# Kernel tuning notes

Measured on AMD Instinct MI355X. Metric: run time of the kernel, lower is better.

Reference implementation:

```python
import jax, jax.numpy as jnp
import numpy as np

B, N, D = 8, 2048, 512

def setup_inputs() -> dict:
    key = jax.random.key(0)
    k1, k2, k3, k4, k5 = jax.random.split(key, 5)
    s = 1.0 / np.sqrt(D)
    return {
        "x": jax.random.normal(k1, (B, N, D), dtype=jnp.float32),
        "w_qkv": jax.random.normal(k2, (D, 3 * D), dtype=jnp.float32) * s,
        "b_qkv": jax.random.normal(k3, (3 * D,), dtype=jnp.float32) * 0.01,
        "w_fc": jax.random.normal(k4, (D, D), dtype=jnp.float32) * s,
        "b_fc": jax.random.normal(k5, (D,), dtype=jnp.float32) * 0.01,
    }

def reference(x, w_qkv, b_qkv, w_fc, b_fc):
    scale = 1.0 / (x.shape[-1] ** 0.5)
    qkv = x @ w_qkv + b_qkv                      # [B, N, 3D]
    q, k, v = jnp.split(qkv, 3, axis=-1)         # each [B, N, D]
    attn = jnp.einsum("bnd,bmd->bnm", q, k) * scale
    attn = jax.nn.softmax(attn, axis=-1)
    out = jnp.einsum("bnm,bmd->bnd", attn, v)
    return out @ w_fc + b_fc + x
```

## Files before the change

kernel.cpp:

```cpp
#include <hip/hip_runtime.h>
#include <stdint.h>

typedef unsigned short u16;
typedef unsigned int u32;
typedef __attribute__((ext_vector_type(8))) short short8;
typedef __attribute__((ext_vector_type(4))) float f32x4;
typedef __attribute__((ext_vector_type(8))) unsigned short u16x8;
typedef __attribute__((ext_vector_type(4))) float float4_t;

__device__ __forceinline__ float b2f(u16 u) { return __uint_as_float(((u32)u) << 16); }
__device__ __forceinline__ u16 f2b(float f) {
  u32 u = __float_as_uint(f);
  u += 0x7fffu + ((u >> 16) & 1u);
  return (u16)(u >> 16);
}

typedef const __attribute__((address_space(1))) void* gas_t;
typedef __attribute__((address_space(3))) void* las_t;
__device__ __forceinline__ void gl_lds16(const void* g, void* l) {
  __builtin_amdgcn_global_load_lds((gas_t)(uintptr_t)g, (las_t)(u32)(uintptr_t)l, 16, 0, 0);
}
__device__ __forceinline__ void barrier_pin() {
  __builtin_amdgcn_sched_barrier(0);
  __builtin_amdgcn_s_barrier();
  __builtin_amdgcn_sched_barrier(0);
}
__device__ __forceinline__ void lgkm0_pin() {
  asm volatile("s_waitcnt lgkmcnt(0)" ::: "memory");
  __builtin_amdgcn_sched_barrier(0);
}

__global__ __launch_bounds__(256) void cvt_f2b_kernel(const float* __restrict__ src,
                                                      u16* __restrict__ dst, long n) {
  long i = ((long)blockIdx.x * 256 + threadIdx.x) * 8;
  if (i >= n) return;
  float4_t v0 = *(const float4_t*)(src + i);
  float4_t v1 = *(const float4_t*)(src + i + 4);
  u16x8 o;
#pragma unroll
  for (int j = 0; j < 4; ++j) { o[j] = f2b(v0[j]); o[4 + j] = f2b(v1[j]); }
  *(u16x8*)(dst + i) = o;
}

__global__ __launch_bounds__(256) void tr_cvt2(const float* __restrict__ w1,
                                               u16* __restrict__ d1,
                                               const float* __restrict__ w2,
                                               u16* __restrict__ d2) {
  const int zz = blockIdx.z;
  if (zz == 1 && blockIdx.x >= 16) return;
  const float* src = zz ? w2 : w1;
  u16* dst = zz ? d2 : d1;
  const int C = zz ? 512 : 1536;
  const int R = 512;
  __shared__ float t[32][33];
  const int bx = blockIdx.x * 32;
  const int by = blockIdx.y * 32;
  const int tx = threadIdx.x & 31, ty = threadIdx.x >> 5;
#pragma unroll
  for (int i = 0; i < 32; i += 8)
    t[ty + i][tx] = src[(long)(by + ty + i) * C + bx + tx];
  __syncthreads();
#pragma unroll
  for (int i = 0; i < 32; i += 8)
    dst[(long)(bx + ty + i) * R + by + tx] = f2b(t[tx][ty + i]);
}

__global__ __launch_bounds__(512) void tr_v(const u16* __restrict__ qkv,
                                            u16* __restrict__ vt) {
  __shared__ u16 t[64][66];
  const int b = blockIdx.z;
  const int r0 = blockIdx.x * 64;
  const int d0 = blockIdx.y * 64;
  const int tr = threadIdx.x >> 3;
  const int tc = (threadIdx.x & 7) * 8;
  *(u16x8*)&t[tr][tc] =
      *(const u16x8*)&qkv[((long)b * 2048 + r0 + tr) * 1536 + 1024 + d0 + tc];
  __syncthreads();
  u16x8 o;
#pragma unroll
  for (int j = 0; j < 8; ++j) o[j] = t[tc + j][tr];
  *(u16x8*)&vt[((long)b * 512 + d0 + tr) * 2048 + r0 + tc] = o;
}

template <bool OUT_F32, bool BIAS, bool RES, bool EXP_EPI, bool ROWSUM_ST, bool DIVROW>
__global__ __launch_bounds__(512, 4)
void gemm128(const u16* __restrict__ A, const u16* __restrict__ Bt, void* __restrict__ Cv,
             const float* __restrict__ bias, const float* __restrict__ res,
             float* __restrict__ lglob, const float* __restrict__ lin,
             int K, int lda, int ldb, int ldc,
             long aStride, long bStride, long cStride, float alpha) {
  __shared__ u16 As[2][128 * 64];
  __shared__ u16 Bs[2][128 * 64];
  const int tid = threadIdx.x;
  const int wid = tid >> 6, lane = tid & 63;
  const int wr = wid >> 2, wc = wid & 3;
  const int lr = lane & 15, lg = lane >> 4;

  const int gx = gridDim.x, gy = gridDim.y;
  int id = (blockIdx.z * gy + blockIdx.y) * gx + blockIdx.x;
  const int nwg = gx * gy * gridDim.z;
  id = (id & 7) * (nwg >> 3) + (id >> 3);
  const int bxi = id % gx;
  const int t2 = id / gx;
  const int byi = t2 % gy;
  const long z = t2 / gy;

  A += z * aStride;
  Bt += z * bStride;
  const int by = byi * 128;
  const int bx = bxi * 128;

  const bool do_l = ROWSUM_ST && (bxi == 0);

  f32x4 acc[4][2] = {};
  f32x4 acc_l[4] = {};
  short8 ah[4][2], bh[2][2];
  short8 ones;
#pragma unroll
  for (int j = 0; j < 8; ++j) ones[j] = (short)0x3F80;

  const int w8l = wid * 8 + (lane >> 3);
  const int scol_src = ((lane & 7) ^ (lane >> 3)) * 8;
  const int scol_lin = (lane & 7) * 8;
  const int nT = K >> 6;
  const int sx = lane & 7;

  auto stage = [&](int kt) {
    const int bb = kt & 1;
    const long kc = (long)kt * 64 + scol_src;
#pragma unroll
    for (int r = 0; r < 2; ++r) {
      const int row = r * 64 + w8l;
      gl_lds16(A + (long)(by + row) * lda + kc, &As[bb][row * 64 + scol_lin]);
    }
#pragma unroll
    for (int r = 0; r < 2; ++r) {
      const int row = r * 64 + w8l;
      gl_lds16(Bt + (long)(bx + row) * ldb + kc, &Bs[bb][row * 64 + scol_lin]);
    }
  };

  stage(0);
  asm volatile("s_waitcnt vmcnt(0)" ::: "memory");
  barrier_pin();

  for (int T = 0; T < nT; ++T) {
    const int bb = T & 1;
    const bool more = (T + 1) < nT;
    if (more) stage(T + 1);
#pragma unroll
    for (int mi = 0; mi < 4; ++mi)
#pragma unroll
      for (int ks = 0; ks < 2; ++ks)
        ah[mi][ks] = *(const short8*)&As[bb][(wr * 64 + mi * 16 + lr) * 64 +
                                             (((ks * 4 + lg) ^ sx) * 8)];
#pragma unroll
    for (int n = 0; n < 2; ++n)
#pragma unroll
      for (int ks = 0; ks < 2; ++ks)
        bh[n][ks] = *(const short8*)&Bs[bb][(wc * 32 + n * 16 + lr) * 64 +
                                            (((ks * 4 + lg) ^ sx) * 8)];
    lgkm0_pin();
    __builtin_amdgcn_s_setprio(1);
#pragma unroll
    for (int mi = 0; mi < 4; ++mi)
#pragma unroll
      for (int n = 0; n < 2; ++n)
#pragma unroll
        for (int ks = 0; ks < 2; ++ks)
          acc[mi][n] = __builtin_amdgcn_mfma_f32_16x16x32_bf16(
              ah[mi][ks], bh[n][ks], acc[mi][n], 0, 0, 0);
    if constexpr (ROWSUM_ST) {
      if (do_l && wc == 0) {
#pragma unroll
        for (int mi = 0; mi < 4; ++mi)
#pragma unroll
          for (int ks = 0; ks < 2; ++ks)
            acc_l[mi] = __builtin_amdgcn_mfma_f32_16x16x32_bf16(
                ah[mi][ks], ones, acc_l[mi], 0, 0, 0);
      }
    }
    __builtin_amdgcn_s_setprio(0);
    if (more) asm volatile("s_waitcnt vmcnt(0)" ::: "memory");
    barrier_pin();
  }

  if constexpr (ROWSUM_ST) {
    if (do_l && wc == 0 && lr == 0) {
#pragma unroll
      for (int mi = 0; mi < 4; ++mi)
#pragma unroll
        for (int j = 0; j < 4; ++j)
          lglob[z * 2048 + by + wr * 64 + mi * 16 + lg * 4 + j] = acc_l[mi][j];
    }
  }

  if constexpr (EXP_EPI) {
    u16* C = (u16*)Cv + z * cStride;
#pragma unroll
    for (int mi = 0; mi < 4; ++mi)
#pragma unroll
      for (int ni = 0; ni < 2; ++ni)
#pragma unroll
        for (int j = 0; j < 4; ++j) {
          const long row = by + wr * 64 + mi * 16 + lg * 4 + j;
          const int col = bx + wc * 32 + ni * 16 + lr;
          C[row * (long)ldc + col] = f2b(exp2f(acc[mi][ni][j] * alpha));
        }
  } else if constexpr (OUT_F32) {
    float* C = (float*)Cv + z * cStride;
#pragma unroll
    for (int mi = 0; mi < 4; ++mi)
#pragma unroll
      for (int j = 0; j < 4; ++j) {
        const long row = by + wr * 64 + mi * 16 + lg * 4 + j;
        float invl = 1.0f;
        if constexpr (DIVROW) invl = 1.0f / lin[row];
#pragma unroll
        for (int ni = 0; ni < 2; ++ni) {
          const int col = bx + wc * 32 + ni * 16 + lr;
          float v = acc[mi][ni][j] * alpha;
          if constexpr (DIVROW) v = acc[mi][ni][j] * invl;
          if (BIAS) v += bias[col];
          if (RES) v += res[row * (long)ldc + col];
          C[row * (long)ldc + col] = v;
        }
      }
  } else {
    u16* C = (u16*)Cv + z * cStride;
#pragma unroll
    for (int mi = 0; mi < 4; ++mi)
#pragma unroll
      for (int ni = 0; ni < 2; ++ni)
#pragma unroll
        for (int j = 0; j < 4; ++j) {
          const long row = by + wr * 64 + mi * 16 + lg * 4 + j;
          const int col = bx + wc * 32 + ni * 16 + lr;
          float v = acc[mi][ni][j] * alpha;
          if (BIAS) v += bias[col];
          C[row * (long)ldc + col] = f2b(v);
        }
  }
}

extern "C" void kernel_launch(void* const* d_in, const int* in_sizes, int n_in,
                              void* d_out, int out_size, void* d_ws, size_t ws_size,
                              hipStream_t stream) {
  const float* x = (const float*)d_in[0];
  const float* w_qkv = (const float*)d_in[1];
  const float* b_qkv = (const float*)d_in[2];
  const float* w_fc = (const float*)d_in[3];
  const float* b_fc = (const float*)d_in[4];
  float* out = (float*)d_out;

  char* ws = (char*)d_ws;
  const long MT = 16384;
  u16* xb = (u16*)(ws);
  u16* wqkvT = (u16*)(ws + 16777216);
  u16* wfcT = (u16*)(ws + 18350080);
  u16* qkv = (u16*)(ws + 18874368);
  u16* vt = (u16*)(ws + 69206016);
  u16* S = (u16*)(ws + 85983232);
  u16* attn = xb;
  float* lvec = (float*)(ws + 16777216);

  const float alpha2 = 0.04419417382415922f * 1.4426950408889634f;

  cvt_f2b_kernel<<<4096, 256, 0, stream>>>(x, xb, MT * 512);
  tr_cvt2<<<dim3(48, 16, 2), 256, 0, stream>>>(w_qkv, wqkvT, w_fc, wfcT);

  gemm128<false, true, false, false, false, false><<<dim3(12, 128, 1), 512, 0, stream>>>(
      xb, wqkvT, qkv, b_qkv, nullptr, nullptr, nullptr,
      512, 512, 512, 1536, 0, 0, 0, 1.0f);

  tr_v<<<dim3(32, 8, 8), 512, 0, stream>>>(qkv, vt);

  gemm128<false, false, false, true, false, false><<<dim3(16, 16, 8), 512, 0, stream>>>(
      qkv, qkv + 512, S, nullptr, nullptr, nullptr, nullptr,
      512, 1536, 1536, 2048,
      (long)2048 * 1536, (long)2048 * 1536, (long)2048 * 2048, alpha2);

  gemm128<false, false, false, false, true, false><<<dim3(4, 16, 8), 512, 0, stream>>>(
      S, vt, attn, nullptr, nullptr, lvec, nullptr,
      2048, 2048, 2048, 512,
      (long)2048 * 2048, (long)512 * 2048, (long)2048 * 512, 1.0f);

  gemm128<true, true, true, false, false, true><<<dim3(4, 128, 1), 512, 0, stream>>>(
      attn, wfcT, out, b_fc, x, nullptr, lvec,
      512, 512, 512, 512, 0, 0, 0, 1.0f);
}
```

Baseline: 160.3 us.

## Switch GEMM tiles to 32x32x16 MFMA and merge preprocessing kernels

Each wave's 64x32 sub-tile now uses two 32x32x16 bf16 MFMA accumulators instead of eight 16x16x32 ones. This cuts the MFMA instruction count and the number of LDS fragment reads per k-step, and the epilogue row/column mapping is rewritten to match the 32x32 output layout. Separately, the x conversion and the weight transpose-convert kernels are merged into one launch to save launch overhead. The risk is a different LDS bank access pattern and a less coalesced epilogue, where each thread now writes 16 scattered rows per column.

```diff
diff --git a/kernel.cpp b/kernel.cpp
--- a/kernel.cpp
+++ b/kernel.cpp
@@ -4,7 +4,7 @@
 typedef unsigned short u16;
 typedef unsigned int u32;
 typedef __attribute__((ext_vector_type(8))) short short8;
-typedef __attribute__((ext_vector_type(4))) float f32x4;
+typedef __attribute__((ext_vector_type(16))) float f32x16;
 typedef __attribute__((ext_vector_type(8))) unsigned short u16x8;
 typedef __attribute__((ext_vector_type(4))) float float4_t;
 
@@ -30,31 +30,36 @@
   __builtin_amdgcn_sched_barrier(0);
 }
 
-__global__ __launch_bounds__(256) void cvt_f2b_kernel(const float* __restrict__ src,
-                                                      u16* __restrict__ dst, long n) {
-  long i = ((long)blockIdx.x * 256 + threadIdx.x) * 8;
-  if (i >= n) return;
-  float4_t v0 = *(const float4_t*)(src + i);
-  float4_t v1 = *(const float4_t*)(src + i + 4);
-  u16x8 o;
-#pragma unroll
-  for (int j = 0; j < 4; ++j) { o[j] = f2b(v0[j]); o[4 + j] = f2b(v1[j]); }
-  *(u16x8*)(dst + i) = o;
-}
-
-__global__ __launch_bounds__(256) void tr_cvt2(const float* __restrict__ w1,
-                                               u16* __restrict__ d1,
-                                               const float* __restrict__ w2,
-                                               u16* __restrict__ d2) {
-  const int zz = blockIdx.z;
-  if (zz == 1 && blockIdx.x >= 16) return;
+__global__ __launch_bounds__(256) void preprocess(const float* __restrict__ x,
+                                                  u16* __restrict__ xb,
+                                                  const float* __restrict__ w1,
+                                                  u16* __restrict__ d1,
+                                                  const float* __restrict__ w2,
+                                                  u16* __restrict__ d2) {
+  const int id = blockIdx.x;
+  if (id < 4096) {
+    long i = ((long)id * 256 + threadIdx.x) * 8;
+    float4_t v0 = *(const float4_t*)(x + i);
+    float4_t v1 = *(const float4_t*)(x + i + 4);
+    u16x8 o;
+#pragma unroll
+    for (int j = 0; j < 4; ++j) { o[j] = f2b(v0[j]); o[4 + j] = f2b(v1[j]); }
+    *(u16x8*)(xb + i) = o;
+    return;
+  }
+  const int rid = id - 4096;
+  const int zz = rid / 768;
+  const int rem = rid - zz * 768;
+  const int bxx = rem % 48;
+  const int byy = rem / 48;
+  if (zz == 1 && bxx >= 16) return;
   const float* src = zz ? w2 : w1;
   u16* dst = zz ? d2 : d1;
   const int C = zz ? 512 : 1536;
   const int R = 512;
   __shared__ float t[32][33];
-  const int bx = blockIdx.x * 32;
-  const int by = blockIdx.y * 32;
+  const int bx = bxx * 32;
+  const int by = byy * 32;
   const int tx = threadIdx.x & 31, ty = threadIdx.x >> 5;
 #pragma unroll
   for (int i = 0; i < 32; i += 8)
@@ -94,7 +99,7 @@
   const int tid = threadIdx.x;
   const int wid = tid >> 6, lane = tid & 63;
   const int wr = wid >> 2, wc = wid & 3;
-  const int lr = lane & 15, lg = lane >> 4;
+  const int l31 = lane & 31, lg2 = lane >> 5;
 
   const int gx = gridDim.x, gy = gridDim.y;
   int id = (blockIdx.z * gy + blockIdx.y) * gx + blockIdx.x;
@@ -112,9 +117,9 @@
 
   const bool do_l = ROWSUM_ST && (bxi == 0);
 
-  f32x4 acc[4][2] = {};
-  f32x4 acc_l[4] = {};
-  short8 ah[4][2], bh[2][2];
+  f32x16 acc[2] = {};
+  f32x16 acc_l[2] = {};
+  short8 ah[2][4], bh[4];
   short8 ones;
 #pragma unroll
   for (int j = 0; j < 8; ++j) ones[j] = (short)0x3F80;
@@ -149,35 +154,31 @@
     const bool more = (T + 1) < nT;
     if (more) stage(T + 1);
 #pragma unroll
-    for (int mi = 0; mi < 4; ++mi)
-#pragma unroll
-      for (int ks = 0; ks < 2; ++ks)
-        ah[mi][ks] = *(const short8*)&As[bb][(wr * 64 + mi * 16 + lr) * 64 +
-                                             (((ks * 4 + lg) ^ sx) * 8)];
-#pragma unroll
-    for (int n = 0; n < 2; ++n)
-#pragma unroll
-      for (int ks = 0; ks < 2; ++ks)
-        bh[n][ks] = *(const short8*)&Bs[bb][(wc * 32 + n * 16 + lr) * 64 +
-                                            (((ks * 4 + lg) ^ sx) * 8)];
+    for (int mf = 0; mf < 2; ++mf)
+#pragma unroll
+      for (int kb = 0; kb < 4; ++kb)
+        ah[mf][kb] = *(const short8*)&As[bb][(wr * 64 + mf * 32 + l31) * 64 +
+                                             (((kb * 2 + lg2) ^ sx) * 8)];
+#pragma unroll
+    for (int kb = 0; kb < 4; ++kb)
+      bh[kb] = *(const short8*)&Bs[bb][(wc * 32 + l31) * 64 +
+                                       (((kb * 2 + lg2) ^ sx) * 8)];
     lgkm0_pin();
     __builtin_amdgcn_s_setprio(1);
 #pragma unroll
-    for (int mi = 0; mi < 4; ++mi)
-#pragma unroll
-      for (int n = 0; n < 2; ++n)
-#pragma unroll
-        for (int ks = 0; ks < 2; ++ks)
-          acc[mi][n] = __builtin_amdgcn_mfma_f32_16x16x32_bf16(
-              ah[mi][ks], bh[n][ks], acc[mi][n], 0, 0, 0);
+    for (int kb = 0; kb < 4; ++kb)
+#pragma unroll
+      for (int mf = 0; mf < 2; ++mf)
+        acc[mf] = __builtin_amdgcn_mfma_f32_32x32x16_bf16(
+            ah[mf][kb], bh[kb], acc[mf], 0, 0, 0);
     if constexpr (ROWSUM_ST) {
       if (do_l && wc == 0) {
 #pragma unroll
-        for (int mi = 0; mi < 4; ++mi)
-#pragma unroll
-          for (int ks = 0; ks < 2; ++ks)
-            acc_l[mi] = __builtin_amdgcn_mfma_f32_16x16x32_bf16(
-                ah[mi][ks], ones, acc_l[mi], 0, 0, 0);
+        for (int kb = 0; kb < 4; ++kb)
+#pragma unroll
+          for (int mf = 0; mf < 2; ++mf)
+            acc_l[mf] = __builtin_amdgcn_mfma_f32_32x32x16_bf16(
+                ah[mf][kb], ones, acc_l[mf], 0, 0, 0);
       }
     }
     __builtin_amdgcn_s_setprio(0);
@@ -185,61 +186,52 @@
     barrier_pin();
   }
 
+  const int col = bx + wc * 32 + l31;
   if constexpr (ROWSUM_ST) {
-    if (do_l && wc == 0 && lr == 0) {
-#pragma unroll
-      for (int mi = 0; mi < 4; ++mi)
-#pragma unroll
-        for (int j = 0; j < 4; ++j)
-          lglob[z * 2048 + by + wr * 64 + mi * 16 + lg * 4 + j] = acc_l[mi][j];
+    if (do_l && wc == 0 && l31 == 0) {
+#pragma unroll
+      for (int mf = 0; mf < 2; ++mf)
+#pragma unroll
+        for (int reg = 0; reg < 16; ++reg)
+          lglob[z * 2048 + by + wr * 64 + mf * 32 + (reg & 3) + 8 * (reg >> 2) + 4 * lg2] =
+              acc_l[mf][reg];
     }
   }
 
   if constexpr (EXP_EPI) {
     u16* C = (u16*)Cv + z * cStride;
 #pragma unroll
-    for (int mi = 0; mi < 4; ++mi)
-#pragma unroll
-      for (int ni = 0; ni < 2; ++ni)
-#pragma unroll
-        for (int j = 0; j < 4; ++j) {
-          const long row = by + wr * 64 + mi * 16 + lg * 4 + j;
-          const int col = bx + wc * 32 + ni * 16 + lr;
-          C[row * (long)ldc + col] = f2b(exp2f(acc[mi][ni][j] * alpha));
-        }
+    for (int mf = 0; mf < 2; ++mf)
+#pragma unroll
+      for (int reg = 0; reg < 16; ++reg) {
+        const long row = by + wr * 64 + mf * 32 + (reg & 3) + 8 * (reg >> 2) + 4 * lg2;
+        C[row * (long)ldc + col] = f2b(exp2f(acc[mf][reg] * alpha));
+      }
   } else if constexpr (OUT_F32) {
     float* C = (float*)Cv + z * cStride;
 #pragma unroll
-    for (int mi = 0; mi < 4; ++mi)
-#pragma unroll
-      for (int j = 0; j < 4; ++j) {
-        const long row = by + wr * 64 + mi * 16 + lg * 4 + j;
-        float invl = 1.0f;
-        if constexpr (DIVROW) invl = 1.0f / lin[row];
-#pragma unroll
-        for (int ni = 0; ni < 2; ++ni) {
-          const int col = bx + wc * 32 + ni * 16 + lr;
-          float v = acc[mi][ni][j] * alpha;
-          if constexpr (DIVROW) v = acc[mi][ni][j] * invl;
-          if (BIAS) v += bias[col];
-          if (RES) v += res[row * (long)ldc + col];
-          C[row * (long)ldc + col] = v;
-        }
+    for (int mf = 0; mf < 2; ++mf)
+#pragma unroll
+      for (int reg = 0; reg < 16; ++reg) {
+        const long row = by + wr * 64 + mf * 32 + (reg & 3) + 8 * (reg >> 2) + 4 * lg2;
+        float v;
+        if constexpr (DIVROW) v = acc[mf][reg] * (1.0f / lin[row]);
+        else                  v = acc[mf][reg] * alpha;
+        if (BIAS) v += bias[col];
+        if (RES) v += res[row * (long)ldc + col];
+        C[row * (long)ldc + col] = v;
       }
   } else {
     u16* C = (u16*)Cv + z * cStride;
 #pragma unroll
-    for (int mi = 0; mi < 4; ++mi)
-#pragma unroll
-      for (int ni = 0; ni < 2; ++ni)
-#pragma unroll
-        for (int j = 0; j < 4; ++j) {
-          const long row = by + wr * 64 + mi * 16 + lg * 4 + j;
-          const int col = bx + wc * 32 + ni * 16 + lr;
-          float v = acc[mi][ni][j] * alpha;
-          if (BIAS) v += bias[col];
-          C[row * (long)ldc + col] = f2b(v);
-        }
+    for (int mf = 0; mf < 2; ++mf)
+#pragma unroll
+      for (int reg = 0; reg < 16; ++reg) {
+        const long row = by + wr * 64 + mf * 32 + (reg & 3) + 8 * (reg >> 2) + 4 * lg2;
+        float v = acc[mf][reg] * alpha;
+        if (BIAS) v += bias[col];
+        C[row * (long)ldc + col] = f2b(v);
+      }
   }
 }
 
@@ -266,8 +258,7 @@
 
   const float alpha2 = 0.04419417382415922f * 1.4426950408889634f;
 
-  cvt_f2b_kernel<<<4096, 256, 0, stream>>>(x, xb, MT * 512);
-  tr_cvt2<<<dim3(48, 16, 2), 256, 0, stream>>>(w_qkv, wqkvT, w_fc, wfcT);
+  preprocess<<<4096 + 1536, 256, 0, stream>>>(x, xb, w_qkv, wqkvT, w_fc, wfcT);
 
   gemm128<false, true, false, false, false, false><<<dim3(12, 128, 1), 512, 0, stream>>>(
       xb, wqkvT, qkv, b_qkv, nullptr, nullptr, nullptr,
```

Result: slower. 188.2 us (+17.4%).
